# Kernel optimization log

Measured on AMD Instinct MI355X. Metric: run time of the kernel, lower is better.

Reference implementation:

```python
import jax, jax.numpy as jnp
import numpy as np

F, N, H = 1024, 16, 64  # features, num_heads, head_dim
B, T, S = 2, 1024, 2048  # batch, query len, memory (kv) len
M = S + 1                # relative position embeddings length


def _relative_shift(x):
    # x: [B, N, T, M] -> [B, N, T, M-1]  (Transformer-XL relative shift)
    b, h, q_len, k_len = x.shape
    x = jnp.pad(x, ((0, 0), (0, 0), (0, 0), (1, 0)))
    x = x.reshape(b, h, k_len + 1, q_len)
    x = x[:, :, 1:, :]
    x = x.reshape(b, h, q_len, k_len)
    return x[..., :-1]


def setup_inputs() -> dict:
    key = jax.random.key(0)
    ks = jax.random.split(key, 12)
    s = 1.0 / np.sqrt(F)
    return {
        'x': jax.random.normal(ks[0], (B, T, F), jnp.float32),
        'rel': jax.random.normal(ks[1], (M, F), jnp.float32),
        'memory': jax.random.normal(ks[2], (B, S, F), jnp.float32),
        'Wq': jax.random.normal(ks[3], (F, N, H), jnp.float32) * s,
        'Wk': jax.random.normal(ks[4], (F, N, H), jnp.float32) * s,
        'Wv': jax.random.normal(ks[5], (F, N, H), jnp.float32) * s,
        'Wr': jax.random.normal(ks[6], (F, N, H), jnp.float32) * s,
        'u_bias': jnp.zeros((N, H), jnp.float32),
        'v_bias': jnp.zeros((N, H), jnp.float32),
        'Wout': jax.random.normal(ks[7], (N * H, F), jnp.float32) * (1.0 / np.sqrt(N * H)),
        'b_out': jnp.zeros((F,), jnp.float32),
    }


def reference(x, rel, memory, Wq, Wk, Wv, Wr, u_bias, v_bias, Wout, b_out):
    b, t = x.shape[0], x.shape[1]
    # projections (DenseGeneral, no bias)
    q = jnp.einsum('btf,fnh->btnh', x, Wq)
    k = jnp.einsum('bsf,fnh->bsnh', memory, Wk)
    v = jnp.einsum('bsf,fnh->bsnh', memory, Wv)
    r = jnp.einsum('mf,fnh->mnh', rel, Wr)
    head_dim = q.shape[-1]
    scale = 1.0 / jnp.sqrt(jnp.asarray(head_dim, jnp.float32))
    q_u = q + u_bias[None, None]
    q_v = q + v_bias[None, None]
    # relative position bias, materialized at [B,N,T,M] then shifted
    bd = jnp.einsum('btnh,mnh->bntm', q_v, r)
    bd = _relative_shift(bd)                        # [B,N,T,S]
    bias = (bd * scale).astype(jnp.float32)
    # attention (dot_product_attention math), q/k/v in bf16 per source
    qb = q_u.astype(jnp.bfloat16)
    kb = k.astype(jnp.bfloat16)
    vb = v.astype(jnp.bfloat16)
    logits = jnp.einsum('btnh,bsnh->bnts', qb, kb).astype(jnp.float32) * scale + bias
    probs = jax.nn.softmax(logits, axis=-1)         # fp32 softmax
    out = jnp.einsum('bnts,bsnh->btnh', probs.astype(jnp.bfloat16), vb)
    out = out.astype(jnp.float32).reshape(b, t, -1)  # [B,T,N*H]
    return out @ Wout + b_out
```

## Files before the change

kernel.cpp:

```cpp
#include <hip/hip_runtime.h>
#include <cmath>

#define C_SCALE 0.18033688011112042f

typedef __attribute__((ext_vector_type(8))) short bf16x8;
typedef __attribute__((ext_vector_type(8))) _Float16 half8;
typedef __attribute__((ext_vector_type(4))) _Float16 half4;
typedef __attribute__((ext_vector_type(4))) float f32x4;
typedef __attribute__((ext_vector_type(4))) unsigned short us4;

__device__ inline unsigned short bf16_rne(float f) {
    unsigned u = __builtin_bit_cast(unsigned, f);
    u += 0x7fff + ((u >> 16) & 1);
    return (unsigned short)(u >> 16);
}

__device__ inline void lds_dma16(const _Float16* g, _Float16* l) {
    __builtin_amdgcn_global_load_lds(
        (__attribute__((address_space(1))) void*)(void*)g,
        (__attribute__((address_space(3))) void*)(void*)l, 16, 0, 0);
}

__global__ __launch_bounds__(256) void convert_kernel(
    const float* __restrict__ x, const float* __restrict__ mem,
    const float* __restrict__ rel,
    _Float16* __restrict__ x16, _Float16* __restrict__ mem16,
    _Float16* __restrict__ rel16)
{
    size_t i = ((size_t)blockIdx.x * 256 + threadIdx.x) * 8;
    if (i >= 8389632ull) return;
    const float* src; _Float16* dst; size_t off;
    if (i < 2097152ull)      { src = x;   dst = x16;   off = i; }
    else if (i < 6291456ull) { src = mem; dst = mem16; off = i - 2097152ull; }
    else                     { src = rel; dst = rel16; off = i - 6291456ull; }
    float4 a = *(const float4*)(src + off);
    float4 b = *(const float4*)(src + off + 4);
    half8 h;
    h[0]=(_Float16)a.x; h[1]=(_Float16)a.y; h[2]=(_Float16)a.z; h[3]=(_Float16)a.w;
    h[4]=(_Float16)b.x; h[5]=(_Float16)b.y; h[6]=(_Float16)b.z; h[7]=(_Float16)b.w;
    *(half8*)(dst + off) = h;
}

__global__ __launch_bounds__(256) void transpose_kernel(
    const float* __restrict__ s0, const float* __restrict__ s1,
    const float* __restrict__ s2, const float* __restrict__ s3,
    const float* __restrict__ s4,
    _Float16* __restrict__ d0, _Float16* __restrict__ d1,
    _Float16* __restrict__ d2, _Float16* __restrict__ d3,
    _Float16* __restrict__ d4)
{
    __shared__ _Float16 T[64][72];
    const int z = blockIdx.z;
    const float* src = z == 0 ? s0 : z == 1 ? s1 : z == 2 ? s2 : z == 3 ? s3 : s4;
    _Float16*    dst = z == 0 ? d0 : z == 1 ? d1 : z == 2 ? d2 : z == 3 ? d3 : d4;
    const int tid = threadIdx.x;
    const int r0 = blockIdx.x * 64, c0 = blockIdx.y * 64;
    const int r = tid >> 4, c4 = (tid & 15) * 4;
    #pragma unroll
    for (int rr = 0; rr < 64; rr += 16) {
        float4 v = *(const float4*)(src + (size_t)(r0 + r + rr) * 1024 + c0 + c4);
        T[c4 + 0][r + rr] = (_Float16)v.x;
        T[c4 + 1][r + rr] = (_Float16)v.y;
        T[c4 + 2][r + rr] = (_Float16)v.z;
        T[c4 + 3][r + rr] = (_Float16)v.w;
    }
    __syncthreads();
    const int orow = tid >> 2, seg = (tid & 3) * 16;
    half8 h0 = *(const half8*)&T[orow][seg];
    half8 h1 = *(const half8*)&T[orow][seg + 8];
    *(half8*)(dst + (size_t)(c0 + orow) * 1024 + r0 + seg)     = h0;
    *(half8*)(dst + (size_t)(c0 + orow) * 1024 + r0 + seg + 8) = h1;
}

__global__ __launch_bounds__(256) void proj2_kernel(
    const _Float16* __restrict__ x16, const _Float16* __restrict__ mem16,
    const _Float16* __restrict__ rel16,
    const _Float16* __restrict__ Wqt, const _Float16* __restrict__ Wkt,
    const _Float16* __restrict__ Wvt, const _Float16* __restrict__ Wrt,
    const float* __restrict__ ub, const float* __restrict__ vb,
    unsigned short* __restrict__ qu, _Float16* __restrict__ qv,
    unsigned short* __restrict__ kb, unsigned short* __restrict__ vtb,
    _Float16* __restrict__ rb)
{
    alignas(16) __shared__ _Float16 As[4096];
    alignas(16) __shared__ _Float16 Bs1[4096];
    alignas(16) __shared__ _Float16 Bs2[4096];
    const int tid = threadIdx.x;
    const int lane = tid & 63, w = tid >> 6, c = lane & 15, g = lane >> 4;
    const int bx = blockIdx.x, col0 = blockIdx.y * 64;

    int mode, row0, rowmax;
    const _Float16* Ap; const _Float16* B1p; const _Float16* B2p = nullptr;
    if (bx < 32)       { mode = 0; row0 = bx * 64;        rowmax = 2047; Ap = x16;   B1p = Wqt; }
    else if (bx < 96)  { mode = 1; row0 = (bx - 32) * 64; rowmax = 4095; Ap = mem16; B1p = Wkt; B2p = Wvt; }
    else               { mode = 2; row0 = (bx - 96) * 64; rowmax = 2048; Ap = rel16; B1p = Wrt; }

    const int srow = 16 * w + (lane >> 3);
    const int phys = lane & 7;
    f32x4 acc1[4] = {}, acc2[4] = {};

    for (int k0 = 0; k0 < 1024; k0 += 64) {
        #pragma unroll
        for (int q = 0; q < 2; q++) {
            int row = srow + 8 * q;
            int log = phys ^ (row & 7);
            int ar = row0 + row; if (ar > rowmax) ar = rowmax;
            lds_dma16(Ap + (size_t)ar * 1024 + k0 + log * 8, &As[(16 * w + 8 * q) * 64]);
            lds_dma16(B1p + (size_t)(col0 + row) * 1024 + k0 + log * 8, &Bs1[(16 * w + 8 * q) * 64]);
            if (mode == 1)
                lds_dma16(B2p + (size_t)(col0 + row) * 1024 + k0 + log * 8, &Bs2[(16 * w + 8 * q) * 64]);
        }
        __syncthreads();
        #pragma unroll
        for (int s = 0; s < 2; s++) {
            const int pc = ((4 * s + g) ^ (c & 7)) * 8;
            half8 af = *(const half8*)&As[(16 * w + c) * 64 + pc];
            #pragma unroll
            for (int j = 0; j < 4; j++) {
                half8 b1 = *(const half8*)&Bs1[(16 * j + c) * 64 + pc];
                acc1[j] = __builtin_amdgcn_mfma_f32_16x16x32_f16(af, b1, acc1[j], 0, 0, 0);
                if (mode == 1) {
                    half8 b2 = *(const half8*)&Bs2[(16 * j + c) * 64 + pc];
                    acc2[j] = __builtin_amdgcn_mfma_f32_16x16x32_f16(af, b2, acc2[j], 0, 0, 0);
                }
            }
        }
        __syncthreads();
    }

    #pragma unroll
    for (int j = 0; j < 4; j++) {
        const int cg = col0 + 16 * j + c;
        if (mode == 0) {
            float u = ub[cg], v = vb[cg];
            #pragma unroll
            for (int rg = 0; rg < 4; rg++) {
                int r_g = row0 + 16 * w + g * 4 + rg;
                size_t o = (size_t)r_g * 1024 + cg;
                qu[o] = bf16_rne(acc1[j][rg] + u);
                qv[o] = (_Float16)((acc1[j][rg] + v) * C_SCALE);
            }
        } else if (mode == 1) {
            int rbase = row0 + 16 * w + g * 4;
            us4 pk;
            #pragma unroll
            for (int rg = 0; rg < 4; rg++) {
                kb[(size_t)(rbase + rg) * 1024 + cg] = bf16_rne(acc1[j][rg]);
                pk[rg] = bf16_rne(acc2[j][rg]);
            }
            int b = rbase >> 11, s = rbase & 2047;
            *(us4*)&vtb[((size_t)(b * 16 + (cg >> 6)) * 64 + (cg & 63)) * 2048 + s] = pk;
        } else {
            #pragma unroll
            for (int rg = 0; rg < 4; rg++) {
                int r_g = row0 + 16 * w + g * 4 + rg;
                if (r_g < 2049)
                    rb[((size_t)(cg >> 6) * 2049 + r_g) * 64 + (cg & 63)] = (_Float16)acc1[j][rg];
            }
        }
    }
}

__global__ __launch_bounds__(256) void flash_kernel(
    const unsigned short* __restrict__ qu, const _Float16* __restrict__ qv,
    const unsigned short* __restrict__ kg, const unsigned short* __restrict__ vt,
    const _Float16* __restrict__ rb, float* __restrict__ po, float* __restrict__ pl)
{
    __shared__ unsigned short Ks[64][70];
    __shared__ unsigned short Vs[64][70];
    __shared__ unsigned short Ps[64][70];
    __shared__ _Float16 BDT[128][70];
    const int tid = threadIdx.x;
    const int lane = tid & 63, w = tid >> 6, c = lane & 15, g = lane >> 4;
    const int id = blockIdx.x;
    const int p_pair = id & 127;
    const int t0 = (id >> 7) * 64;
    const int bn = p_pair >> 2, part = p_pair & 3;
    const int b = bn >> 4, n = bn & 15;
    const int s_start = part * 512;

    const unsigned short* qp = qu + (size_t)(b * 1024 + t0 + 16 * w + c) * 1024 + n * 64 + g * 8;
    bf16x8 qf0 = *(const bf16x8*)qp;
    bf16x8 qf1 = *(const bf16x8*)(qp + 32);
    const _Float16* qvp = qv + (size_t)(b * 1024 + t0 + 16 * w + c) * 1024 + n * 64 + g * 8;
    half8 av0 = *(const half8*)qvp;
    half8 av1 = *(const half8*)(qvp + 32);
    int r2 = t0 + 16 * w + c + 1; if (r2 > 1023) r2 = 1023;
    const _Float16* qvp2 = qv + (size_t)(b * 1024 + r2) * 1024 + n * 64 + g * 8;
    half8 aw0 = *(const half8*)qvp2;
    half8 aw1 = *(const half8*)(qvp2 + 32);

    const _Float16* rbase = rb + (size_t)n * 2049 * 64;

    f32x4 o[4] = {};
    float l_i[4] = {0.f, 0.f, 0.f, 0.f};

    const int sr = tid >> 2, scc = (tid & 3) * 16;
    const unsigned short* kstage = kg + (size_t)(b * 2048 + s_start + sr) * 1024 + n * 64 + scc;
    const unsigned short* vstage = vt + ((size_t)bn * 64 + sr) * 2048 + s_start + scc;

    auto bd_tile = [&](int Dbase, int nj) {
        for (int j = 0; j < nj; j++) {
            int Dl = Dbase + 16 * j + c;
            int Dmin = Dbase + 16 * j;
            int mm;
            if (Dl <= 1026) { mm = Dl + 1023; if (mm > 2048) mm = 2048; }
            else mm = Dl - 1027;
            const _Float16* rp = rbase + (size_t)mm * 64 + g * 8;
            half8 rb0 = *(const half8*)rp;
            half8 rb1 = *(const half8*)(rp + 32);
            f32x4 z;
            if (Dmin + 15 <= 1026) {
                f32x4 zm = {};
                zm = __builtin_amdgcn_mfma_f32_16x16x32_f16(av0, rb0, zm, 0, 0, 0);
                zm = __builtin_amdgcn_mfma_f32_16x16x32_f16(av1, rb1, zm, 0, 0, 0);
                z = zm;
            } else if (Dmin >= 1027) {
                f32x4 zw = {};
                zw = __builtin_amdgcn_mfma_f32_16x16x32_f16(aw0, rb0, zw, 0, 0, 0);
                zw = __builtin_amdgcn_mfma_f32_16x16x32_f16(aw1, rb1, zw, 0, 0, 0);
                z = zw;
            } else {
                f32x4 zm = {}, zw = {};
                zm = __builtin_amdgcn_mfma_f32_16x16x32_f16(av0, rb0, zm, 0, 0, 0);
                zm = __builtin_amdgcn_mfma_f32_16x16x32_f16(av1, rb1, zm, 0, 0, 0);
                zw = __builtin_amdgcn_mfma_f32_16x16x32_f16(aw0, rb0, zw, 0, 0, 0);
                zw = __builtin_amdgcn_mfma_f32_16x16x32_f16(aw1, rb1, zw, 0, 0, 0);
                z = (Dl >= 1027) ? zw : zm;
            }
            if (Dl == 1026) { z[0] = 0.f; z[1] = 0.f; z[2] = 0.f; z[3] = 0.f; }
            half4 hv;
            #pragma unroll
            for (int rg = 0; rg < 4; rg++) hv[rg] = (_Float16)z[rg];
            *(half4*)&BDT[Dl & 127][16 * w + 4 * g] = hv;
        }
    };

    for (int kk = 0; kk < 8; kk++) {
        const int s0 = s_start + kk * 64;
        const int diff0 = s0 - t0;

        *(uint4*)&Ks[sr][scc]     = *(const uint4*)(kstage + (size_t)(kk * 64) * 1024);
        *(uint4*)&Ks[sr][scc + 8] = *(const uint4*)(kstage + (size_t)(kk * 64) * 1024 + 8);
        *(uint4*)&Vs[sr][scc]     = *(const uint4*)(vstage + kk * 64);
        *(uint4*)&Vs[sr][scc + 8] = *(const uint4*)(vstage + kk * 64 + 8);

        if (kk == 0) bd_tile(diff0 - 63, 8);
        else         bd_tile(diff0 + 1, 4);

        __syncthreads();

        #pragma unroll
        for (int j = 0; j < 4; j++) {
            bf16x8 kf0 = *(const bf16x8*)&Ks[16 * j + c][g * 8];
            bf16x8 kf1 = *(const bf16x8*)&Ks[16 * j + c][32 + g * 8];
            f32x4 sa = {};
            sa = __builtin_amdgcn_mfma_f32_16x16x32_bf16(qf0, kf0, sa, 0, 0, 0);
            sa = __builtin_amdgcn_mfma_f32_16x16x32_bf16(qf1, kf1, sa, 0, 0, 0);
            #pragma unroll
            for (int rg = 0; rg < 4; rg++) {
                int tt = 16 * w + 4 * g + rg;
                int D = diff0 + 16 * j + c - tt;
                float bdt = (float)BDT[D & 127][tt];
                float p = exp2f(fmaf(sa[rg], C_SCALE, bdt));
                l_i[rg] += p;
                Ps[tt][16 * j + c] = bf16_rne(p);
            }
        }

        bf16x8 pf0 = *(const bf16x8*)&Ps[16 * w + c][g * 8];
        bf16x8 pf1 = *(const bf16x8*)&Ps[16 * w + c][32 + g * 8];
        #pragma unroll
        for (int j = 0; j < 4; j++) {
            bf16x8 vf0 = *(const bf16x8*)&Vs[16 * j + c][g * 8];
            bf16x8 vf1 = *(const bf16x8*)&Vs[16 * j + c][32 + g * 8];
            o[j] = __builtin_amdgcn_mfma_f32_16x16x32_bf16(pf0, vf0, o[j], 0, 0, 0);
            o[j] = __builtin_amdgcn_mfma_f32_16x16x32_bf16(pf1, vf1, o[j], 0, 0, 0);
        }
        __syncthreads();
    }

    #pragma unroll
    for (int rg = 0; rg < 4; rg++) {
        float s2 = l_i[rg];
        #pragma unroll
        for (int off = 1; off < 16; off <<= 1)
            s2 += __shfl_xor(s2, off, 16);
        int t = t0 + 16 * w + 4 * g + rg;
        size_t rowb = ((size_t)part * 32 + bn) * 1024 + t;
        if (c == 0) pl[rowb] = s2;
        #pragma unroll
        for (int j = 0; j < 4; j++)
            po[rowb * 64 + 16 * j + c] = o[j][rg];
    }
}

__global__ __launch_bounds__(256) void combine_kernel(
    const float* __restrict__ po, const float* __restrict__ pl,
    _Float16* __restrict__ attn)
{
    int f = blockIdx.x * 256 + threadIdx.x;
    int h = f & 63, t = (f >> 6) & 1023, bn = f >> 16;
    float os = 0.f, ls = 0.f;
    #pragma unroll
    for (int p = 0; p < 4; p++) {
        size_t rowb = ((size_t)p * 32 + bn) * 1024 + t;
        os += po[rowb * 64 + h];
        ls += pl[rowb];
    }
    int b = bn >> 4, n = bn & 15;
    attn[((size_t)b * 1024 + t) * 1024 + n * 64 + h] = (_Float16)(os / ls);
}

__global__ __launch_bounds__(256) void out2_kernel(
    const _Float16* __restrict__ A, const _Float16* __restrict__ Bt,
    const float* __restrict__ bias, float* __restrict__ out)
{
    alignas(16) __shared__ _Float16 As[4096];
    alignas(16) __shared__ _Float16 Bs[4096];
    const int tid = threadIdx.x;
    const int lane = tid & 63, w = tid >> 6, c = lane & 15, g = lane >> 4;
    const int row0 = blockIdx.x * 64, col0 = blockIdx.y * 64;
    const int srow = 16 * w + (lane >> 3);
    const int phys = lane & 7;
    f32x4 acc[4] = {};

    for (int k0 = 0; k0 < 1024; k0 += 64) {
        #pragma unroll
        for (int q = 0; q < 2; q++) {
            int row = srow + 8 * q;
            int log = phys ^ (row & 7);
            lds_dma16(A  + (size_t)(row0 + row) * 1024 + k0 + log * 8, &As[(16 * w + 8 * q) * 64]);
            lds_dma16(Bt + (size_t)(col0 + row) * 1024 + k0 + log * 8, &Bs[(16 * w + 8 * q) * 64]);
        }
        __syncthreads();
        #pragma unroll
        for (int s = 0; s < 2; s++) {
            const int pc = ((4 * s + g) ^ (c & 7)) * 8;
            half8 af = *(const half8*)&As[(16 * w + c) * 64 + pc];
            #pragma unroll
            for (int j = 0; j < 4; j++) {
                half8 bf = *(const half8*)&Bs[(16 * j + c) * 64 + pc];
                acc[j] = __builtin_amdgcn_mfma_f32_16x16x32_f16(af, bf, acc[j], 0, 0, 0);
            }
        }
        __syncthreads();
    }
    #pragma unroll
    for (int j = 0; j < 4; j++)
        #pragma unroll
        for (int rg = 0; rg < 4; rg++) {
            int r_g = row0 + 16 * w + g * 4 + rg, cg = col0 + 16 * j + c;
            out[(size_t)r_g * 1024 + cg] = acc[j][rg] + bias[cg];
        }
}

extern "C" void kernel_launch(void* const* d_in, const int* in_sizes, int n_in,
                              void* d_out, int out_size, void* d_ws, size_t ws_size,
                              hipStream_t stream)
{
    const float* x    = (const float*)d_in[0];
    const float* rel  = (const float*)d_in[1];
    const float* mem  = (const float*)d_in[2];
    const float* Wq   = (const float*)d_in[3];
    const float* Wk   = (const float*)d_in[4];
    const float* Wv   = (const float*)d_in[5];
    const float* Wr   = (const float*)d_in[6];
    const float* ub   = (const float*)d_in[7];
    const float* vb   = (const float*)d_in[8];
    const float* Wout = (const float*)d_in[9];
    const float* bout = (const float*)d_in[10];
    float* out = (float*)d_out;

    char* ws = (char*)d_ws;
    unsigned short* qu    = (unsigned short*)(ws);
    _Float16*       qv    = (_Float16*)(ws + (4ull << 20));
    unsigned short* kb    = (unsigned short*)(ws + (8ull << 20));
    unsigned short* vtb   = (unsigned short*)(ws + (16ull << 20));
    _Float16*       rb    = (_Float16*)(ws + (24ull << 20));
    _Float16*       attn  = (_Float16*)(ws + (29ull << 20));
    float*          po    = (float*)(ws + (33ull << 20));
    float*          pl    = (float*)(ws + (68ull << 20));
    _Float16*       x16   = (_Float16*)(ws + (69ull << 20));
    _Float16*       mem16 = (_Float16*)(ws + (73ull << 20));
    _Float16*       rel16 = (_Float16*)(ws + (81ull << 20));
    _Float16*       Wqt   = (_Float16*)(ws + (86ull << 20));
    _Float16*       Wkt   = (_Float16*)(ws + (88ull << 20));
    _Float16*       Wvt   = (_Float16*)(ws + (90ull << 20));
    _Float16*       Wrt   = (_Float16*)(ws + (92ull << 20));
    _Float16*       Woutt = (_Float16*)(ws + (94ull << 20));

    convert_kernel<<<dim3(4097), 256, 0, stream>>>(x, mem, rel, x16, mem16, rel16);
    transpose_kernel<<<dim3(16, 16, 5), 256, 0, stream>>>(
        Wq, Wk, Wv, Wr, Wout, Wqt, Wkt, Wvt, Wrt, Woutt);
    proj2_kernel<<<dim3(129, 16), 256, 0, stream>>>(
        x16, mem16, rel16, Wqt, Wkt, Wvt, Wrt, ub, vb, qu, qv, kb, vtb, rb);
    flash_kernel<<<dim3(2048), 256, 0, stream>>>(qu, qv, kb, vtb, rb, po, pl);
    combine_kernel<<<dim3(8192), 256, 0, stream>>>(po, pl, attn);
    out2_kernel<<<dim3(32, 16), 256, 0, stream>>>(attn, Woutt, bout, out);
}
```

Measured before the change: 320.0 us.

## Merge prep kernels, enlarge projection tiles, prefetch flash loads, store fp16 partials

Merges the fp32-to-fp16 conversion and weight transpose into one launch and reworks the projection GEMM into 128x128 tiles with a 4x4 MFMA register block per wave, giving K and V separate blocks. The flash kernel now prefetches the next K/V tile and the relative-position rows into registers while the current tile is computed. It also writes normalized partial outputs as fp16 instead of fp32, so the combine kernel reads half the bytes. These changes cut launch overhead, raise reuse in the GEMM and overlap load latency. The cost is more register pressure and lower precision in the partial outputs.

```diff
diff --git a/kernel.cpp b/kernel.cpp
--- a/kernel.cpp
+++ b/kernel.cpp
@@ -21,58 +21,57 @@
         (__attribute__((address_space(3))) void*)(void*)l, 16, 0, 0);
 }
 
-__global__ __launch_bounds__(256) void convert_kernel(
+__global__ __launch_bounds__(256) void prep_kernel(
     const float* __restrict__ x, const float* __restrict__ mem,
     const float* __restrict__ rel,
-    _Float16* __restrict__ x16, _Float16* __restrict__ mem16,
-    _Float16* __restrict__ rel16)
-{
-    size_t i = ((size_t)blockIdx.x * 256 + threadIdx.x) * 8;
-    if (i >= 8389632ull) return;
-    const float* src; _Float16* dst; size_t off;
-    if (i < 2097152ull)      { src = x;   dst = x16;   off = i; }
-    else if (i < 6291456ull) { src = mem; dst = mem16; off = i - 2097152ull; }
-    else                     { src = rel; dst = rel16; off = i - 6291456ull; }
-    float4 a = *(const float4*)(src + off);
-    float4 b = *(const float4*)(src + off + 4);
-    half8 h;
-    h[0]=(_Float16)a.x; h[1]=(_Float16)a.y; h[2]=(_Float16)a.z; h[3]=(_Float16)a.w;
-    h[4]=(_Float16)b.x; h[5]=(_Float16)b.y; h[6]=(_Float16)b.z; h[7]=(_Float16)b.w;
-    *(half8*)(dst + off) = h;
-}
-
-__global__ __launch_bounds__(256) void transpose_kernel(
     const float* __restrict__ s0, const float* __restrict__ s1,
     const float* __restrict__ s2, const float* __restrict__ s3,
     const float* __restrict__ s4,
+    _Float16* __restrict__ x16, _Float16* __restrict__ mem16,
+    _Float16* __restrict__ rel16,
     _Float16* __restrict__ d0, _Float16* __restrict__ d1,
     _Float16* __restrict__ d2, _Float16* __restrict__ d3,
     _Float16* __restrict__ d4)
 {
-    __shared__ _Float16 T[64][72];
-    const int z = blockIdx.z;
-    const float* src = z == 0 ? s0 : z == 1 ? s1 : z == 2 ? s2 : z == 3 ? s3 : s4;
-    _Float16*    dst = z == 0 ? d0 : z == 1 ? d1 : z == 2 ? d2 : z == 3 ? d3 : d4;
-    const int tid = threadIdx.x;
-    const int r0 = blockIdx.x * 64, c0 = blockIdx.y * 64;
-    const int r = tid >> 4, c4 = (tid & 15) * 4;
-    #pragma unroll
-    for (int rr = 0; rr < 64; rr += 16) {
-        float4 v = *(const float4*)(src + (size_t)(r0 + r + rr) * 1024 + c0 + c4);
-        T[c4 + 0][r + rr] = (_Float16)v.x;
-        T[c4 + 1][r + rr] = (_Float16)v.y;
-        T[c4 + 2][r + rr] = (_Float16)v.z;
-        T[c4 + 3][r + rr] = (_Float16)v.w;
-    }
-    __syncthreads();
-    const int orow = tid >> 2, seg = (tid & 3) * 16;
-    half8 h0 = *(const half8*)&T[orow][seg];
-    half8 h1 = *(const half8*)&T[orow][seg + 8];
-    *(half8*)(dst + (size_t)(c0 + orow) * 1024 + r0 + seg)     = h0;
-    *(half8*)(dst + (size_t)(c0 + orow) * 1024 + r0 + seg + 8) = h1;
-}
-
-__global__ __launch_bounds__(256) void proj2_kernel(
+    const int bx = blockIdx.x, tid = threadIdx.x;
+    if (bx < 1280) {
+        __shared__ _Float16 T[64][72];
+        const int z = bx >> 8, rem = bx & 255;
+        const float* src = z == 0 ? s0 : z == 1 ? s1 : z == 2 ? s2 : z == 3 ? s3 : s4;
+        _Float16*    dst = z == 0 ? d0 : z == 1 ? d1 : z == 2 ? d2 : z == 3 ? d3 : d4;
+        const int r0 = (rem & 15) * 64, c0 = (rem >> 4) * 64;
+        const int r = tid >> 4, c4 = (tid & 15) * 4;
+        #pragma unroll
+        for (int rr = 0; rr < 64; rr += 16) {
+            float4 v = *(const float4*)(src + (size_t)(r0 + r + rr) * 1024 + c0 + c4);
+            T[c4 + 0][r + rr] = (_Float16)v.x;
+            T[c4 + 1][r + rr] = (_Float16)v.y;
+            T[c4 + 2][r + rr] = (_Float16)v.z;
+            T[c4 + 3][r + rr] = (_Float16)v.w;
+        }
+        __syncthreads();
+        const int orow = tid >> 2, seg = (tid & 3) * 16;
+        half8 h0 = *(const half8*)&T[orow][seg];
+        half8 h1 = *(const half8*)&T[orow][seg + 8];
+        *(half8*)(dst + (size_t)(c0 + orow) * 1024 + r0 + seg)     = h0;
+        *(half8*)(dst + (size_t)(c0 + orow) * 1024 + r0 + seg + 8) = h1;
+    } else {
+        size_t i = ((size_t)(bx - 1280) * 256 + tid) * 8;
+        if (i >= 8389632ull) return;
+        const float* src; _Float16* dst; size_t off;
+        if (i < 2097152ull)      { src = x;   dst = x16;   off = i; }
+        else if (i < 6291456ull) { src = mem; dst = mem16; off = i - 2097152ull; }
+        else                     { src = rel; dst = rel16; off = i - 6291456ull; }
+        float4 a = *(const float4*)(src + off);
+        float4 b = *(const float4*)(src + off + 4);
+        half8 h;
+        h[0]=(_Float16)a.x; h[1]=(_Float16)a.y; h[2]=(_Float16)a.z; h[3]=(_Float16)a.w;
+        h[4]=(_Float16)b.x; h[5]=(_Float16)b.y; h[6]=(_Float16)b.z; h[7]=(_Float16)b.w;
+        *(half8*)(dst + off) = h;
+    }
+}
+
+__global__ __launch_bounds__(256) void proj3_kernel(
     const _Float16* __restrict__ x16, const _Float16* __restrict__ mem16,
     const _Float16* __restrict__ rel16,
     const _Float16* __restrict__ Wqt, const _Float16* __restrict__ Wkt,
@@ -82,80 +81,86 @@
     unsigned short* __restrict__ kb, unsigned short* __restrict__ vtb,
     _Float16* __restrict__ rb)
 {
-    alignas(16) __shared__ _Float16 As[4096];
-    alignas(16) __shared__ _Float16 Bs1[4096];
-    alignas(16) __shared__ _Float16 Bs2[4096];
+    alignas(16) __shared__ _Float16 As[128 * 64];
+    alignas(16) __shared__ _Float16 Bs[128 * 64];
     const int tid = threadIdx.x;
     const int lane = tid & 63, w = tid >> 6, c = lane & 15, g = lane >> 4;
-    const int bx = blockIdx.x, col0 = blockIdx.y * 64;
+    const int bx = blockIdx.x, col0 = blockIdx.y * 128;
 
     int mode, row0, rowmax;
-    const _Float16* Ap; const _Float16* B1p; const _Float16* B2p = nullptr;
-    if (bx < 32)       { mode = 0; row0 = bx * 64;        rowmax = 2047; Ap = x16;   B1p = Wqt; }
-    else if (bx < 96)  { mode = 1; row0 = (bx - 32) * 64; rowmax = 4095; Ap = mem16; B1p = Wkt; B2p = Wvt; }
-    else               { mode = 2; row0 = (bx - 96) * 64; rowmax = 2048; Ap = rel16; B1p = Wrt; }
-
-    const int srow = 16 * w + (lane >> 3);
-    const int phys = lane & 7;
-    f32x4 acc1[4] = {}, acc2[4] = {};
+    const _Float16 *Ap, *Bp;
+    if (bx < 16)      { mode = 0; row0 = bx * 128;        rowmax = 2047; Ap = x16;   Bp = Wqt; }
+    else if (bx < 48) { mode = 1; row0 = (bx - 16) * 128; rowmax = 4095; Ap = mem16; Bp = Wkt; }
+    else if (bx < 80) { mode = 2; row0 = (bx - 48) * 128; rowmax = 4095; Ap = mem16; Bp = Wvt; }
+    else              { mode = 3; row0 = (bx - 80) * 128; rowmax = 2048; Ap = rel16; Bp = Wrt; }
+
+    const int qr = (w & 1) * 64, qc = (w >> 1) * 64;
+    const int srow = lane >> 3, phys = lane & 7;
+    f32x4 acc[4][4] = {};
 
     for (int k0 = 0; k0 < 1024; k0 += 64) {
         #pragma unroll
-        for (int q = 0; q < 2; q++) {
-            int row = srow + 8 * q;
+        for (int q = 0; q < 4; q++) {
+            int row = 32 * w + 8 * q + srow;
             int log = phys ^ (row & 7);
             int ar = row0 + row; if (ar > rowmax) ar = rowmax;
-            lds_dma16(Ap + (size_t)ar * 1024 + k0 + log * 8, &As[(16 * w + 8 * q) * 64]);
-            lds_dma16(B1p + (size_t)(col0 + row) * 1024 + k0 + log * 8, &Bs1[(16 * w + 8 * q) * 64]);
-            if (mode == 1)
-                lds_dma16(B2p + (size_t)(col0 + row) * 1024 + k0 + log * 8, &Bs2[(16 * w + 8 * q) * 64]);
+            lds_dma16(Ap + (size_t)ar * 1024 + k0 + log * 8, &As[(32 * w + 8 * q) * 64]);
+            lds_dma16(Bp + (size_t)(col0 + row) * 1024 + k0 + log * 8, &Bs[(32 * w + 8 * q) * 64]);
         }
         __syncthreads();
         #pragma unroll
         for (int s = 0; s < 2; s++) {
-            const int pc = ((4 * s + g) ^ (c & 7)) * 8;
-            half8 af = *(const half8*)&As[(16 * w + c) * 64 + pc];
+            half8 af[4], bf[4];
+            #pragma unroll
+            for (int i = 0; i < 4; i++) {
+                int row = qr + 16 * i + c;
+                af[i] = *(const half8*)&As[row * 64 + ((4 * s + g) ^ (row & 7)) * 8];
+            }
             #pragma unroll
             for (int j = 0; j < 4; j++) {
-                half8 b1 = *(const half8*)&Bs1[(16 * j + c) * 64 + pc];
-                acc1[j] = __builtin_amdgcn_mfma_f32_16x16x32_f16(af, b1, acc1[j], 0, 0, 0);
-                if (mode == 1) {
-                    half8 b2 = *(const half8*)&Bs2[(16 * j + c) * 64 + pc];
-                    acc2[j] = __builtin_amdgcn_mfma_f32_16x16x32_f16(af, b2, acc2[j], 0, 0, 0);
+                int row = qc + 16 * j + c;
+                bf[j] = *(const half8*)&Bs[row * 64 + ((4 * s + g) ^ (row & 7)) * 8];
+            }
+            #pragma unroll
+            for (int i = 0; i < 4; i++)
+                #pragma unroll
+                for (int j = 0; j < 4; j++)
+                    acc[i][j] = __builtin_amdgcn_mfma_f32_16x16x32_f16(af[i], bf[j], acc[i][j], 0, 0, 0);
+        }
+        __syncthreads();
+    }
+
+    #pragma unroll
+    for (int i = 0; i < 4; i++) {
+        #pragma unroll
+        for (int j = 0; j < 4; j++) {
+            const int cg = col0 + qc + 16 * j + c;
+            const int rbase = row0 + qr + 16 * i + 4 * g;
+            if (mode == 0) {
+                float u = ub[cg], v = vb[cg];
+                #pragma unroll
+                for (int rg = 0; rg < 4; rg++) {
+                    size_t o = (size_t)(rbase + rg) * 1024 + cg;
+                    qu[o] = bf16_rne(acc[i][j][rg] + u);
+                    qv[o] = (_Float16)((acc[i][j][rg] + v) * C_SCALE);
                 }
-            }
-        }
-        __syncthreads();
-    }
-
-    #pragma unroll
-    for (int j = 0; j < 4; j++) {
-        const int cg = col0 + 16 * j + c;
-        if (mode == 0) {
-            float u = ub[cg], v = vb[cg];
-            #pragma unroll
-            for (int rg = 0; rg < 4; rg++) {
-                int r_g = row0 + 16 * w + g * 4 + rg;
-                size_t o = (size_t)r_g * 1024 + cg;
-                qu[o] = bf16_rne(acc1[j][rg] + u);
-                qv[o] = (_Float16)((acc1[j][rg] + v) * C_SCALE);
-            }
-        } else if (mode == 1) {
-            int rbase = row0 + 16 * w + g * 4;
-            us4 pk;
-            #pragma unroll
-            for (int rg = 0; rg < 4; rg++) {
-                kb[(size_t)(rbase + rg) * 1024 + cg] = bf16_rne(acc1[j][rg]);
-                pk[rg] = bf16_rne(acc2[j][rg]);
-            }
-            int b = rbase >> 11, s = rbase & 2047;
-            *(us4*)&vtb[((size_t)(b * 16 + (cg >> 6)) * 64 + (cg & 63)) * 2048 + s] = pk;
-        } else {
-            #pragma unroll
-            for (int rg = 0; rg < 4; rg++) {
-                int r_g = row0 + 16 * w + g * 4 + rg;
-                if (r_g < 2049)
-                    rb[((size_t)(cg >> 6) * 2049 + r_g) * 64 + (cg & 63)] = (_Float16)acc1[j][rg];
+            } else if (mode == 1) {
+                #pragma unroll
+                for (int rg = 0; rg < 4; rg++)
+                    kb[(size_t)(rbase + rg) * 1024 + cg] = bf16_rne(acc[i][j][rg]);
+            } else if (mode == 2) {
+                us4 pk;
+                #pragma unroll
+                for (int rg = 0; rg < 4; rg++) pk[rg] = bf16_rne(acc[i][j][rg]);
+                int b = rbase >> 11, s = rbase & 2047;
+                *(us4*)&vtb[((size_t)(b * 16 + (cg >> 6)) * 64 + (cg & 63)) * 2048 + s] = pk;
+            } else {
+                #pragma unroll
+                for (int rg = 0; rg < 4; rg++) {
+                    int r_g = rbase + rg;
+                    if (r_g < 2049)
+                        rb[((size_t)(cg >> 6) * 2049 + r_g) * 64 + (cg & 63)] = (_Float16)acc[i][j][rg];
+                }
             }
         }
     }
@@ -164,7 +169,7 @@
 __global__ __launch_bounds__(256) void flash_kernel(
     const unsigned short* __restrict__ qu, const _Float16* __restrict__ qv,
     const unsigned short* __restrict__ kg, const unsigned short* __restrict__ vt,
-    const _Float16* __restrict__ rb, float* __restrict__ po, float* __restrict__ pl)
+    const _Float16* __restrict__ rb, _Float16* __restrict__ po, float* __restrict__ pl)
 {
     __shared__ unsigned short Ks[64][70];
     __shared__ unsigned short Vs[64][70];
@@ -199,56 +204,83 @@
     const unsigned short* kstage = kg + (size_t)(b * 2048 + s_start + sr) * 1024 + n * 64 + scc;
     const unsigned short* vstage = vt + ((size_t)bn * 64 + sr) * 2048 + s_start + scc;
 
-    auto bd_tile = [&](int Dbase, int nj) {
-        for (int j = 0; j < nj; j++) {
-            int Dl = Dbase + 16 * j + c;
-            int Dmin = Dbase + 16 * j;
-            int mm;
-            if (Dl <= 1026) { mm = Dl + 1023; if (mm > 2048) mm = 2048; }
-            else mm = Dl - 1027;
-            const _Float16* rp = rbase + (size_t)mm * 64 + g * 8;
-            half8 rb0 = *(const half8*)rp;
-            half8 rb1 = *(const half8*)(rp + 32);
-            f32x4 z;
-            if (Dmin + 15 <= 1026) {
-                f32x4 zm = {};
-                zm = __builtin_amdgcn_mfma_f32_16x16x32_f16(av0, rb0, zm, 0, 0, 0);
-                zm = __builtin_amdgcn_mfma_f32_16x16x32_f16(av1, rb1, zm, 0, 0, 0);
-                z = zm;
-            } else if (Dmin >= 1027) {
-                f32x4 zw = {};
-                zw = __builtin_amdgcn_mfma_f32_16x16x32_f16(aw0, rb0, zw, 0, 0, 0);
-                zw = __builtin_amdgcn_mfma_f32_16x16x32_f16(aw1, rb1, zw, 0, 0, 0);
-                z = zw;
-            } else {
-                f32x4 zm = {}, zw = {};
-                zm = __builtin_amdgcn_mfma_f32_16x16x32_f16(av0, rb0, zm, 0, 0, 0);
-                zm = __builtin_amdgcn_mfma_f32_16x16x32_f16(av1, rb1, zm, 0, 0, 0);
-                zw = __builtin_amdgcn_mfma_f32_16x16x32_f16(aw0, rb0, zw, 0, 0, 0);
-                zw = __builtin_amdgcn_mfma_f32_16x16x32_f16(aw1, rb1, zw, 0, 0, 0);
-                z = (Dl >= 1027) ? zw : zm;
-            }
-            if (Dl == 1026) { z[0] = 0.f; z[1] = 0.f; z[2] = 0.f; z[3] = 0.f; }
-            half4 hv;
-            #pragma unroll
-            for (int rg = 0; rg < 4; rg++) hv[rg] = (_Float16)z[rg];
-            *(half4*)&BDT[Dl & 127][16 * w + 4 * g] = hv;
-        }
+    auto r_ptr = [&](int Dl) {
+        int mm = (Dl <= 1026) ? (Dl + 1023 > 2048 ? 2048 : Dl + 1023) : Dl - 1027;
+        return rbase + (size_t)mm * 64 + g * 8;
     };
+    auto bd_one = [&](int Dbase, int j, half8 r0, half8 r1) {
+        int Dl = Dbase + 16 * j + c;
+        int Dmin = Dbase + 16 * j;
+        f32x4 z;
+        if (Dmin + 15 <= 1026) {
+            f32x4 zm = {};
+            zm = __builtin_amdgcn_mfma_f32_16x16x32_f16(av0, r0, zm, 0, 0, 0);
+            zm = __builtin_amdgcn_mfma_f32_16x16x32_f16(av1, r1, zm, 0, 0, 0);
+            z = zm;
+        } else if (Dmin >= 1027) {
+            f32x4 zw = {};
+            zw = __builtin_amdgcn_mfma_f32_16x16x32_f16(aw0, r0, zw, 0, 0, 0);
+            zw = __builtin_amdgcn_mfma_f32_16x16x32_f16(aw1, r1, zw, 0, 0, 0);
+            z = zw;
+        } else {
+            f32x4 zm = {}, zw = {};
+            zm = __builtin_amdgcn_mfma_f32_16x16x32_f16(av0, r0, zm, 0, 0, 0);
+            zm = __builtin_amdgcn_mfma_f32_16x16x32_f16(av1, r1, zm, 0, 0, 0);
+            zw = __builtin_amdgcn_mfma_f32_16x16x32_f16(aw0, r0, zw, 0, 0, 0);
+            zw = __builtin_amdgcn_mfma_f32_16x16x32_f16(aw1, r1, zw, 0, 0, 0);
+            z = (Dl >= 1027) ? zw : zm;
+        }
+        if (Dl == 1026) { z[0] = 0.f; z[1] = 0.f; z[2] = 0.f; z[3] = 0.f; }
+        half4 hv;
+        #pragma unroll
+        for (int rg = 0; rg < 4; rg++) hv[rg] = (_Float16)z[rg];
+        *(half4*)&BDT[Dl & 127][16 * w + 4 * g] = hv;
+    };
+
+    const int d0 = s_start - t0;
+    half8 rx[8], rr[8];
+    #pragma unroll
+    for (int j = 0; j < 4; j++) {
+        const _Float16* rp = r_ptr(d0 - 63 + 16 * j + c);
+        rx[2 * j] = *(const half8*)rp; rx[2 * j + 1] = *(const half8*)(rp + 32);
+    }
+    #pragma unroll
+    for (int j = 0; j < 4; j++) {
+        const _Float16* rp = r_ptr(d0 + 1 + 16 * j + c);
+        rr[2 * j] = *(const half8*)rp; rr[2 * j + 1] = *(const half8*)(rp + 32);
+    }
+    uint4 k0r = *(const uint4*)(kstage);
+    uint4 k1r = *(const uint4*)(kstage + 8);
+    uint4 v0r = *(const uint4*)(vstage);
+    uint4 v1r = *(const uint4*)(vstage + 8);
 
     for (int kk = 0; kk < 8; kk++) {
-        const int s0 = s_start + kk * 64;
-        const int diff0 = s0 - t0;
-
-        *(uint4*)&Ks[sr][scc]     = *(const uint4*)(kstage + (size_t)(kk * 64) * 1024);
-        *(uint4*)&Ks[sr][scc + 8] = *(const uint4*)(kstage + (size_t)(kk * 64) * 1024 + 8);
-        *(uint4*)&Vs[sr][scc]     = *(const uint4*)(vstage + kk * 64);
-        *(uint4*)&Vs[sr][scc + 8] = *(const uint4*)(vstage + kk * 64 + 8);
-
-        if (kk == 0) bd_tile(diff0 - 63, 8);
-        else         bd_tile(diff0 + 1, 4);
-
-        __syncthreads();
+        const int diff0 = d0 + kk * 64;
+
+        *(uint4*)&Ks[sr][scc]     = k0r;
+        *(uint4*)&Ks[sr][scc + 8] = k1r;
+        *(uint4*)&Vs[sr][scc]     = v0r;
+        *(uint4*)&Vs[sr][scc + 8] = v1r;
+        if (kk == 0) {
+            #pragma unroll
+            for (int j = 0; j < 4; j++) bd_one(d0 - 63, j, rx[2 * j], rx[2 * j + 1]);
+        }
+        #pragma unroll
+        for (int j = 0; j < 4; j++) bd_one(diff0 + 1, j, rr[2 * j], rr[2 * j + 1]);
+
+        __syncthreads();
+
+        const int kn = kk < 7 ? kk + 1 : 7;
+        k0r = *(const uint4*)(kstage + (size_t)(kn * 64) * 1024);
+        k1r = *(const uint4*)(kstage + (size_t)(kn * 64) * 1024 + 8);
+        v0r = *(const uint4*)(vstage + kn * 64);
+        v1r = *(const uint4*)(vstage + kn * 64 + 8);
+        const int Dn = diff0 + 65;
+        #pragma unroll
+        for (int j = 0; j < 4; j++) {
+            const _Float16* rp = r_ptr(Dn + 16 * j + c);
+            rr[2 * j] = *(const half8*)rp; rr[2 * j + 1] = *(const half8*)(rp + 32);
+        }
 
         #pragma unroll
         for (int j = 0; j < 4; j++) {
@@ -289,14 +321,15 @@
         int t = t0 + 16 * w + 4 * g + rg;
         size_t rowb = ((size_t)part * 32 + bn) * 1024 + t;
         if (c == 0) pl[rowb] = s2;
+        float inv = 1.f / s2;
         #pragma unroll
         for (int j = 0; j < 4; j++)
-            po[rowb * 64 + 16 * j + c] = o[j][rg];
+            po[rowb * 64 + 16 * j + c] = (_Float16)(o[j][rg] * inv);
     }
 }
 
 __global__ __launch_bounds__(256) void combine_kernel(
-    const float* __restrict__ po, const float* __restrict__ pl,
+    const _Float16* __restrict__ po, const float* __restrict__ pl,
     _Float16* __restrict__ attn)
 {
     int f = blockIdx.x * 256 + threadIdx.x;
@@ -305,8 +338,9 @@
     #pragma unroll
     for (int p = 0; p < 4; p++) {
         size_t rowb = ((size_t)p * 32 + bn) * 1024 + t;
-        os += po[rowb * 64 + h];
-        ls += pl[rowb];
+        float lp = pl[rowb];
+        os += lp * (float)po[rowb * 64 + h];
+        ls += lp;
     }
     int b = bn >> 4, n = bn & 15;
     attn[((size_t)b * 1024 + t) * 1024 + n * 64 + h] = (_Float16)(os / ls);
@@ -379,21 +413,21 @@
     unsigned short* vtb   = (unsigned short*)(ws + (16ull << 20));
     _Float16*       rb    = (_Float16*)(ws + (24ull << 20));
     _Float16*       attn  = (_Float16*)(ws + (29ull << 20));
-    float*          po    = (float*)(ws + (33ull << 20));
-    float*          pl    = (float*)(ws + (68ull << 20));
-    _Float16*       x16   = (_Float16*)(ws + (69ull << 20));
-    _Float16*       mem16 = (_Float16*)(ws + (73ull << 20));
-    _Float16*       rel16 = (_Float16*)(ws + (81ull << 20));
-    _Float16*       Wqt   = (_Float16*)(ws + (86ull << 20));
-    _Float16*       Wkt   = (_Float16*)(ws + (88ull << 20));
-    _Float16*       Wvt   = (_Float16*)(ws + (90ull << 20));
-    _Float16*       Wrt   = (_Float16*)(ws + (92ull << 20));
-    _Float16*       Woutt = (_Float16*)(ws + (94ull << 20));
-
-    convert_kernel<<<dim3(4097), 256, 0, stream>>>(x, mem, rel, x16, mem16, rel16);
-    transpose_kernel<<<dim3(16, 16, 5), 256, 0, stream>>>(
-        Wq, Wk, Wv, Wr, Wout, Wqt, Wkt, Wvt, Wrt, Woutt);
-    proj2_kernel<<<dim3(129, 16), 256, 0, stream>>>(
+    _Float16*       po    = (_Float16*)(ws + (33ull << 20));
+    float*          pl    = (float*)(ws + (50ull << 20));
+    _Float16*       x16   = (_Float16*)(ws + (51ull << 20));
+    _Float16*       mem16 = (_Float16*)(ws + (55ull << 20));
+    _Float16*       rel16 = (_Float16*)(ws + (63ull << 20));
+    _Float16*       Wqt   = (_Float16*)(ws + (68ull << 20));
+    _Float16*       Wkt   = (_Float16*)(ws + (70ull << 20));
+    _Float16*       Wvt   = (_Float16*)(ws + (72ull << 20));
+    _Float16*       Wrt   = (_Float16*)(ws + (74ull << 20));
+    _Float16*       Woutt = (_Float16*)(ws + (76ull << 20));
+
+    prep_kernel<<<dim3(5377), 256, 0, stream>>>(
+        x, mem, rel, Wq, Wk, Wv, Wr, Wout,
+        x16, mem16, rel16, Wqt, Wkt, Wvt, Wrt, Woutt);
+    proj3_kernel<<<dim3(97, 8), 256, 0, stream>>>(
         x16, mem16, rel16, Wqt, Wkt, Wvt, Wrt, ub, vb, qu, qv, kb, vtb, rb);
     flash_kernel<<<dim3(2048), 256, 0, stream>>>(qu, qv, kb, vtb, rb, po, pl);
     combine_kernel<<<dim3(8192), 256, 0, stream>>>(po, pl, attn);
```

Result: faster. 280.3 us (-12.4%).
